# Kernel optimization log

Measured on AMD Instinct MI355X. Metric: run time of the kernel, lower is better.

The kernel has to match this reference:

```python
import jax, jax.numpy as jnp
import numpy as np

NUM_CLASSES = 512
WIDTH = 2  # triangular half-width in bins
MODE = 'triangular'
SIGMA = 1.0
B = 65536


def setup_inputs() -> dict:
    key = jax.random.key(0)
    k1, k2 = jax.random.split(key)
    logits = jax.random.normal(k1, (B, NUM_CLASSES), dtype=jnp.float32)
    targets = jax.random.randint(k2, (B,), 0, NUM_CLASSES, dtype=jnp.int64)
    return {"logits": logits, "targets": targets}


def _soft_targets(targets, C, dtype):
    # Vectorized replacement of the per-row Python loop.
    c = targets[:, None]                     # [B, 1]
    j = jnp.arange(C)[None, :]               # [1, C]
    d = jnp.abs(j - c)                       # [B, C] bin distance
    if MODE == 'triangular':
        w = jnp.where(d <= WIDTH, (WIDTH + 1 - d).astype(dtype), jnp.zeros((), dtype))
    elif MODE == 'log-triangular':
        w = jnp.where(d <= WIDTH, jnp.exp(-d.astype(dtype)), jnp.zeros((), dtype))
    else:  # gaussian
        w = jnp.where(d <= WIDTH,
                      jnp.exp(-0.5 * (d.astype(dtype) / SIGMA) ** 2),
                      jnp.zeros((), dtype))
    return w / jnp.sum(w, axis=1, keepdims=True)


def reference(logits, targets):
    Bsz, C = logits.shape
    st = _soft_targets(targets, C, logits.dtype)        # [B, C] normalized soft labels
    logp = jax.nn.log_softmax(logits, axis=1)            # [B, C]
    # KL(st || softmax(logits)) with 0*log0 = 0, matching F.kl_div(log_probs, st)
    safe_st = jnp.where(st > 0, st, jnp.ones((), logits.dtype))
    kl = jnp.where(st > 0, st * (jnp.log(safe_st) - logp), jnp.zeros((), logits.dtype))
    return jnp.sum(kl) / Bsz  # batchmean
```

## Files before the change

kernel.cpp:

```cpp
#include <hip/hip_runtime.h>

#define CDIM 512
#define BROWS 65536
#define NBLK 16384

typedef float floatx4 __attribute__((ext_vector_type(4)));

__device__ __forceinline__ float wpart(int j, int t, float x) {
    int d = j - t;
    int ad = d < 0 ? -d : d;
    return (ad <= 2) ? (float)(3 - ad) * x : 0.0f;
}

__global__ __launch_bounds__(256) void SoftTargetLoss_62646392979666_kernel(
        const float* __restrict__ logits,
        const int* __restrict__ targets,
        float* __restrict__ partials) {
    const int lane = threadIdx.x & 63;
    const int wid  = threadIdx.x >> 6;
    const int row  = blockIdx.x * 4 + wid;

    const floatx4* rp = (const floatx4*)(logits + (size_t)row * CDIM);
    floatx4 a = __builtin_nontemporal_load(rp + lane);
    floatx4 b = __builtin_nontemporal_load(rp + lane + 64);
    const int tt = targets[row];

    float s = __expf(a.x) + __expf(a.y) + __expf(a.z) + __expf(a.w)
            + __expf(b.x) + __expf(b.y) + __expf(b.z) + __expf(b.w);

    const int j0 = lane * 4, j1 = 256 + lane * 4;
    float dp = wpart(j0,     tt, a.x) + wpart(j0 + 1, tt, a.y)
             + wpart(j0 + 2, tt, a.z) + wpart(j0 + 3, tt, a.w)
             + wpart(j1,     tt, b.x) + wpart(j1 + 1, tt, b.y)
             + wpart(j1 + 2, tt, b.z) + wpart(j1 + 3, tt, b.w);

    #pragma unroll
    for (int off = 32; off >= 1; off >>= 1) {
        s  += __shfl_xor(s,  off, 64);
        dp += __shfl_xor(dp, off, 64);
    }

    float H, invW;
    if (tt >= 2 && tt <= CDIM - 3) { H = -1.52295508f; invW = 1.0f / 9.0f; }
    else if (tt == 0 || tt == CDIM - 1) { H = -1.01140427f; invW = 1.0f / 6.0f; }
    else { H = -1.32088835f; invW = 1.0f / 8.0f; }

    __shared__ float sred[4];
    if (lane == 0) sred[wid] = H + __logf(s) - dp * invW;
    __syncthreads();
    if (threadIdx.x == 0)
        partials[blockIdx.x] = sred[0] + sred[1] + sred[2] + sred[3];
}

__global__ __launch_bounds__(256) void stl_reduce(
        const float* __restrict__ partials, float* __restrict__ out) {
    const floatx4* p4 = (const floatx4*)partials;
    floatx4 v4 = {0.f, 0.f, 0.f, 0.f};
    #pragma unroll
    for (int i = 0; i < NBLK / 4 / 256; ++i) v4 += p4[threadIdx.x + i * 256];
    float v = v4.x + v4.y + v4.z + v4.w;
    #pragma unroll
    for (int off = 32; off >= 1; off >>= 1) v += __shfl_xor(v, off, 64);
    __shared__ float sred[4];
    if ((threadIdx.x & 63) == 0) sred[threadIdx.x >> 6] = v;
    __syncthreads();
    if (threadIdx.x == 0)
        out[0] = (sred[0] + sred[1] + sred[2] + sred[3]) * (1.0f / (float)BROWS);
}

extern "C" void kernel_launch(void* const* d_in, const int* in_sizes, int n_in,
                              void* d_out, int out_size, void* d_ws, size_t ws_size,
                              hipStream_t stream) {
    const float* logits   = (const float*)d_in[0];
    const int*   targets  = (const int*)d_in[1];
    float*       out      = (float*)d_out;
    float*       partials = (float*)d_ws;

    SoftTargetLoss_62646392979666_kernel<<<NBLK, 256, 0, stream>>>(logits, targets, partials);
    stl_reduce<<<1, 256, 0, stream>>>(partials, out);
}
```

Baseline: 180.7 us.

## Process multiple rows per wave with software-prefetched loads and deferred dot reduction

Shrinks the grid from 16384 to 2048 blocks so each wave handles 8 consecutive rows in a loop. The next row's logits and target are loaded before the current row is processed, and the weighted dot-product reduction is moved out of the loop into a single shuffle reduction at the end. This cuts block launch overhead, per-block shared-memory reduction work and the size of the partials array. The cost is fewer resident waves to hide memory latency, partly offset by the one-row prefetch.

```diff
diff --git a/kernel.cpp b/kernel.cpp
--- a/kernel.cpp
+++ b/kernel.cpp
@@ -2,7 +2,9 @@
 
 #define CDIM 512
 #define BROWS 65536
-#define NBLK 16384
+#define NBLK 2048
+#define WAVES_TOTAL (NBLK * 4)
+#define RPW (BROWS / WAVES_TOTAL)
 
 typedef float floatx4 __attribute__((ext_vector_type(4)));
 
@@ -12,41 +14,62 @@
     return (ad <= 2) ? (float)(3 - ad) * x : 0.0f;
 }
 
-__global__ __launch_bounds__(256) void SoftTargetLoss_62646392979666_kernel(
+__global__ __launch_bounds__(256, 8) void SoftTargetLoss_62646392979666_kernel(
         const float* __restrict__ logits,
         const int* __restrict__ targets,
         float* __restrict__ partials) {
     const int lane = threadIdx.x & 63;
     const int wid  = threadIdx.x >> 6;
-    const int row  = blockIdx.x * 4 + wid;
+    const int wave = blockIdx.x * 4 + wid;
+    const int row0 = wave * RPW;
+    const int j0 = lane * 4, j1 = 256 + lane * 4;
 
-    const floatx4* rp = (const floatx4*)(logits + (size_t)row * CDIM);
-    floatx4 a = __builtin_nontemporal_load(rp + lane);
-    floatx4 b = __builtin_nontemporal_load(rp + lane + 64);
-    const int tt = targets[row];
+    const floatx4* rp = (const floatx4*)(logits + (size_t)row0 * CDIM) + lane;
 
-    float s = __expf(a.x) + __expf(a.y) + __expf(a.z) + __expf(a.w)
-            + __expf(b.x) + __expf(b.y) + __expf(b.z) + __expf(b.w);
+    floatx4 a = __builtin_nontemporal_load(rp);
+    floatx4 b = __builtin_nontemporal_load(rp + 64);
+    int t = targets[row0];
 
-    const int j0 = lane * 4, j1 = 256 + lane * 4;
-    float dp = wpart(j0,     tt, a.x) + wpart(j0 + 1, tt, a.y)
-             + wpart(j0 + 2, tt, a.z) + wpart(j0 + 3, tt, a.w)
-             + wpart(j1,     tt, b.x) + wpart(j1 + 1, tt, b.y)
-             + wpart(j1 + 2, tt, b.z) + wpart(j1 + 3, tt, b.w);
+    float accU = 0.0f;
+    float dpw  = 0.0f;
+
+    #pragma unroll 1
+    for (int it = 0; it < RPW; ++it) {
+        floatx4 an, bn; int tn;
+        const bool more = (it + 1 < RPW);
+        if (more) {
+            const floatx4* np = rp + (size_t)(it + 1) * (CDIM / 4);
+            an = __builtin_nontemporal_load(np);
+            bn = __builtin_nontemporal_load(np + 64);
+            tn = targets[row0 + it + 1];
+        }
+
+        float s = __expf(a.x) + __expf(a.y) + __expf(a.z) + __expf(a.w)
+                + __expf(b.x) + __expf(b.y) + __expf(b.z) + __expf(b.w);
+        #pragma unroll
+        for (int off = 32; off >= 1; off >>= 1) s += __shfl_xor(s, off, 64);
+
+        float dp = wpart(j0,     t, a.x) + wpart(j0 + 1, t, a.y)
+                 + wpart(j0 + 2, t, a.z) + wpart(j0 + 3, t, a.w)
+                 + wpart(j1,     t, b.x) + wpart(j1 + 1, t, b.y)
+                 + wpart(j1 + 2, t, b.z) + wpart(j1 + 3, t, b.w);
+
+        float H, invW;
+        if (t >= 2 && t <= CDIM - 3)      { H = -1.52295508f; invW = 1.0f / 9.0f; }
+        else if (t == 0 || t == CDIM - 1) { H = -1.01140427f; invW = 1.0f / 6.0f; }
+        else                              { H = -1.32088835f; invW = 1.0f / 8.0f; }
+
+        accU += H + __logf(s);
+        dpw  += dp * invW;
+
+        if (more) { a = an; b = bn; t = tn; }
+    }
 
     #pragma unroll
-    for (int off = 32; off >= 1; off >>= 1) {
-        s  += __shfl_xor(s,  off, 64);
-        dp += __shfl_xor(dp, off, 64);
-    }
-
-    float H, invW;
-    if (tt >= 2 && tt <= CDIM - 3) { H = -1.52295508f; invW = 1.0f / 9.0f; }
-    else if (tt == 0 || tt == CDIM - 1) { H = -1.01140427f; invW = 1.0f / 6.0f; }
-    else { H = -1.32088835f; invW = 1.0f / 8.0f; }
+    for (int off = 32; off >= 1; off >>= 1) dpw += __shfl_xor(dpw, off, 64);
 
     __shared__ float sred[4];
-    if (lane == 0) sred[wid] = H + __logf(s) - dp * invW;
+    if (lane == 0) sred[wid] = accU - dpw;
     __syncthreads();
     if (threadIdx.x == 0)
         partials[blockIdx.x] = sred[0] + sred[1] + sred[2] + sred[3];
@@ -55,9 +78,7 @@
 __global__ __launch_bounds__(256) void stl_reduce(
         const float* __restrict__ partials, float* __restrict__ out) {
     const floatx4* p4 = (const floatx4*)partials;
-    floatx4 v4 = {0.f, 0.f, 0.f, 0.f};
-    #pragma unroll
-    for (int i = 0; i < NBLK / 4 / 256; ++i) v4 += p4[threadIdx.x + i * 256];
+    floatx4 v4 = p4[threadIdx.x] + p4[threadIdx.x + 256];
     float v = v4.x + v4.y + v4.z + v4.w;
     #pragma unroll
     for (int off = 32; off >= 1; off >>= 1) v += __shfl_xor(v, off, 64);
```

After: 182.9 us. Within noise of the previous version (+1.2%).
